# Performance work log

Measured on AMD Instinct MI355X. Metric: run time of the kernel, lower is better.

The kernel has to match this reference:

```python
import jax, jax.numpy as jnp
import numpy as np

LN_EPS = 1e-5


def setup_inputs() -> dict:
    key = jax.random.key(0)
    ks = jax.random.split(key, 8)
    dim = 256
    b, n3 = 8, 6144  # seq dim holds 3 concatenated token streams of n=2048 each
    s = 0.02
    return {
        "x": jax.random.normal(ks[0], (b, n3, dim), jnp.float32),
        "ln_g": jnp.ones((dim,), jnp.float32),
        "ln_b": jnp.zeros((dim,), jnp.float32),
        "Wq": jax.random.normal(ks[1], (dim, dim), jnp.float32) * s,
        "bq": jax.random.normal(ks[2], (dim,), jnp.float32) * s,
        "Wk": jax.random.normal(ks[3], (dim, dim), jnp.float32) * s,
        "bk": jax.random.normal(ks[4], (dim,), jnp.float32) * s,
        "Wv": jax.random.normal(ks[5], (dim, dim), jnp.float32) * s,
        "bv": jax.random.normal(ks[6], (dim,), jnp.float32) * s,
        "Wo": jax.random.normal(ks[7], (dim, dim), jnp.float32) * s,
        "bo": jnp.zeros((dim,), jnp.float32),
        "heads": 8,
    }


def reference(x, ln_g, ln_b, Wq, bq, Wk, bk, Wv, bv, Wo, bo, heads):
    dim = x.shape[-1]
    scale = dim ** (-0.5)  # NOTE: full dim, as in the original module
    d = dim // heads

    def cross_attn(xcat):
        # LayerNorm over last dim (applied to concatenated [2b, n, dim])
        mu = jnp.mean(xcat, axis=-1, keepdims=True)
        var = jnp.mean(jnp.square(xcat - mu), axis=-1, keepdims=True)
        xn = (xcat - mu) * jax.lax.rsqrt(var + LN_EPS) * ln_g + ln_b
        x1, x2 = jnp.split(xn, 2, axis=0)  # queries from stream 1, kv from stream 2
        q = x1 @ Wq.T + bq
        k = x2 @ Wk.T + bk
        v = x2 @ Wv.T + bv
        b_, n_ = q.shape[0], q.shape[1]
        q = q.reshape(b_, n_, heads, d).transpose(0, 2, 1, 3)  # b h n d
        k = k.reshape(b_, n_, heads, d).transpose(0, 2, 1, 3)
        v = v.reshape(b_, n_, heads, d).transpose(0, 2, 1, 3)
        dots = jnp.einsum('bhid,bhjd->bhij', q, k) * scale
        attn = jax.nn.softmax(dots, axis=-1)
        out = jnp.einsum('bhij,bhjd->bhid', attn, v)
        out = out.transpose(0, 2, 1, 3).reshape(b_, n_, dim)
        return out @ Wo.T + bo  # dropout is identity in eval

    x_origin, x_emap, x_lbp = jnp.split(x, 3, axis=1)
    out_oe = cross_attn(jnp.concatenate((x_origin, x_emap), axis=0))
    out_ol = cross_attn(jnp.concatenate((x_origin, x_lbp), axis=0))
    return out_oe + out_ol
```

## Files before the change

### kernel.cpp

```cpp
#include <hip/hip_runtime.h>
#include <hip/hip_bf16.h>
#include <math.h>

#define LN_EPS 1e-5f
#define QSCALE 0.09016844005556021f

typedef __attribute__((ext_vector_type(8))) short short8;
typedef __attribute__((ext_vector_type(4))) short short4v;
typedef __attribute__((ext_vector_type(4))) float f32x4;

__device__ inline ushort f2bf(float f) {
  __hip_bfloat16 h = __float2bfloat16(f);
  return *reinterpret_cast<ushort*>(&h);
}

__device__ inline uint pk2bf(float a, float b) {
  uint ua = __float_as_uint(a) + 0x8000u;
  uint ub = __float_as_uint(b) + 0x8000u;
  return __builtin_amdgcn_perm(ub, ua, 0x07060302u);
}


__global__ __launch_bounds__(256) void ln_wcast_kernel(
    const float* __restrict__ x, const float* __restrict__ lng,
    const float* __restrict__ lnb,
    const float* __restrict__ Wq, const float* __restrict__ Wk,
    const float* __restrict__ Wv, const float* __restrict__ Wo,
    ushort* __restrict__ xn, ushort* __restrict__ wbf) {
  if (blockIdx.x < 256) {
    int t = blockIdx.x * 256 + threadIdx.x;
    int e0 = t * 4;
    int m = e0 >> 16, off = e0 & 65535;
    const float* src = (m == 0) ? Wq : (m == 1) ? Wk : (m == 2) ? Wv : Wo;
    float4 v = *(const float4*)(src + off);
    ushort4 o;
    o.x = f2bf(v.x); o.y = f2bf(v.y); o.z = f2bf(v.z); o.w = f2bf(v.w);
    *(ushort4*)(wbf + m * 65536 + off) = o;
    return;
  }
  int w = threadIdx.x >> 6;
  int lane = threadIdx.x & 63;
  size_t token = (size_t)(blockIdx.x - 256) * 4 + w;
  float4 v = *(const float4*)(x + token * 256 + lane * 4);
  float s  = v.x + v.y + v.z + v.w;
  float s2 = v.x * v.x + v.y * v.y + v.z * v.z + v.w * v.w;
#pragma unroll
  for (int off = 32; off >= 1; off >>= 1) {
    s  += __shfl_xor(s, off, 64);
    s2 += __shfl_xor(s2, off, 64);
  }
  float mu  = s * (1.0f / 256.0f);
  float var = s2 * (1.0f / 256.0f) - mu * mu;
  float rs  = rsqrtf(var + LN_EPS);
  float4 g = *(const float4*)(lng + lane * 4);
  float4 bb = *(const float4*)(lnb + lane * 4);
  ushort4 o;
  o.x = f2bf((v.x - mu) * rs * g.x + bb.x);
  o.y = f2bf((v.y - mu) * rs * g.y + bb.y);
  o.z = f2bf((v.z - mu) * rs * g.z + bb.z);
  o.w = f2bf((v.w - mu) * rs * g.w + bb.w);
  *(ushort4*)(xn + token * 256 + lane * 4) = o;
}

__global__ __launch_bounds__(256) void proj_kernel(
    const ushort* __restrict__ xn,
    const ushort* __restrict__ wq, const ushort* __restrict__ wk,
    const ushort* __restrict__ wv,
    const float* __restrict__ bq, const float* __restrict__ bk,
    const float* __restrict__ bv,
    ushort* __restrict__ qb, ushort* __restrict__ keb, ushort* __restrict__ vTe,
    ushort* __restrict__ klb, ushort* __restrict__ vTl) {
  int z = blockIdx.z;
  const ushort* W; const float* bias; ushort* out; int s; bool isV; float scl;
  if (z == 0)      { W = wq; bias = bq; out = qb;  s = 0; isV = false; scl = QSCALE; }
  else if (z == 1) { W = wk; bias = bk; out = keb; s = 1; isV = false; scl = 1.0f; }
  else if (z == 2) { W = wv; bias = bv; out = vTe; s = 1; isV = true;  scl = 1.0f; }
  else if (z == 3) { W = wk; bias = bk; out = klb; s = 2; isV = false; scl = 1.0f; }
  else             { W = wv; bias = bv; out = vTl; s = 2; isV = true;  scl = 1.0f; }

  int tid = threadIdx.x;
  int w = tid >> 6, lane = tid & 63;
  int n = lane & 15, quad = lane >> 4;
  int cbase = blockIdx.y * 128 + w * 32;

  short8 wfrag[2][8];
#pragma unroll
  for (int ct = 0; ct < 2; ++ct)
#pragma unroll
    for (int kc = 0; kc < 8; ++kc)
      wfrag[ct][kc] = *(const short8*)(W + (size_t)(cbase + ct * 16 + n) * 256 + kc * 32 + quad * 8);
  float4 bt[2]; float bsc[2];
  if (!isV) {
    bt[0] = *(const float4*)(bias + cbase + quad * 4);
    bt[1] = *(const float4*)(bias + cbase + 16 + quad * 4);
  } else {
    bsc[0] = bias[cbase + n];
    bsc[1] = bias[cbase + 16 + n];
  }

  for (int tt = 0; tt < 8; ++tt) {
    int t0 = blockIdx.x * 128 + tt * 16;
    int tok = t0 + n;
    int b = tok >> 11, n2 = tok & 2047;
    const ushort* xrow = xn + ((size_t)b * 6144 + s * 2048 + n2) * 256;
    short8 xf[8];
#pragma unroll
    for (int kc = 0; kc < 8; ++kc)
      xf[kc] = *(const short8*)(xrow + kc * 32 + quad * 8);
    f32x4 acc[2] = {{0.f, 0.f, 0.f, 0.f}, {0.f, 0.f, 0.f, 0.f}};
#pragma unroll
    for (int ct = 0; ct < 2; ++ct)
#pragma unroll
      for (int kc = 0; kc < 8; ++kc)
        acc[ct] = isV
          ? __builtin_amdgcn_mfma_f32_16x16x32_bf16(xf[kc], wfrag[ct][kc], acc[ct], 0, 0, 0)
          : __builtin_amdgcn_mfma_f32_16x16x32_bf16(wfrag[ct][kc], xf[kc], acc[ct], 0, 0, 0);

    if (!isV) {
#pragma unroll
      for (int ct = 0; ct < 2; ++ct) {
        int c = cbase + ct * 16 + quad * 4;
        int h = c >> 5, d = c & 31;
        float* bp = (float*)&bt[ct];
        ushort4 st;
        st.x = f2bf((acc[ct][0] + bp[0]) * scl);
        st.y = f2bf((acc[ct][1] + bp[1]) * scl);
        st.z = f2bf((acc[ct][2] + bp[2]) * scl);
        st.w = f2bf((acc[ct][3] + bp[3]) * scl);
        *(ushort4*)(out + (((size_t)(b * 8 + h) * 2048) + n2) * 32 + d) = st;
      }
    } else {
      int tq0 = t0 + quad * 4;
      int b2 = tq0 >> 11, n2q = tq0 & 2047;
#pragma unroll
      for (int ct = 0; ct < 2; ++ct) {
        int c = cbase + ct * 16 + n;
        int h = c >> 5, d = c & 31;
        ushort4 st;
        st.x = f2bf(acc[ct][0] + bsc[ct]);
        st.y = f2bf(acc[ct][1] + bsc[ct]);
        st.z = f2bf(acc[ct][2] + bsc[ct]);
        st.w = f2bf(acc[ct][3] + bsc[ct]);
        *(ushort4*)(out + (((size_t)(b2 * 8 + h) * 32) + d) * 2048 + n2q) = st;
      }
    }
  }
}

__global__ __launch_bounds__(256) void attn_kernel(
    const ushort* __restrict__ q,
    const ushort* __restrict__ ke, const ushort* __restrict__ vTe,
    const ushort* __restrict__ kl, const ushort* __restrict__ vTl,
    ushort* __restrict__ osum) {
  __shared__ __align__(16) short Vt[4][32 * 72];

  int tid = threadIdx.x;
  int w = tid >> 6, lane = tid & 63;
  int n = lane & 15, quad = lane >> 4;
  short* VtW = &Vt[w][0];

  int L = blockIdx.y * 8 + blockIdx.x;
  int xcd = L & 7, idx = L >> 3;
  int bh = (idx & 7) * 8 + xcd;
  int q0 = (idx >> 3) * 256;
  int qbase = q0 + w * 64;

  short8 qfrag[4];
#pragma unroll
  for (int gq = 0; gq < 4; ++gq)
    qfrag[gq] = *(const short8*)(q + ((size_t)bh * 2048 + qbase + gq * 16 + n) * 32 + quad * 8);

  f32x4 out_acc[4][2];
#pragma unroll
  for (int gq = 0; gq < 4; ++gq)
#pragma unroll
    for (int dh = 0; dh < 2; ++dh) out_acc[gq][dh] = (f32x4){0.f, 0.f, 0.f, 0.f};

  int vrow = lane >> 3, vcol = (lane & 7) * 8;

  for (int s = 0; s < 2; ++s) {
    const ushort* K  = (s == 0 ? ke : kl) + (size_t)bh * 2048 * 32;
    const ushort* VT = (s == 0 ? vTe : vTl) + (size_t)bh * 32 * 2048;
    float lp[4] = {0.f, 0.f, 0.f, 0.f};
    f32x4 oacc[4][2];
#pragma unroll
    for (int gq = 0; gq < 4; ++gq)
#pragma unroll
      for (int dh = 0; dh < 2; ++dh) oacc[gq][dh] = (f32x4){0.f, 0.f, 0.f, 0.f};

    short8 kfc[4], vrc[4], kfn[4], vrn[4];
#pragma unroll
    for (int t4 = 0; t4 < 4; ++t4)
      kfc[t4] = *(const short8*)(K + (size_t)(t4 * 16 + n) * 32 + quad * 8);
#pragma unroll
    for (int it = 0; it < 4; ++it)
      vrc[it] = *(const short8*)(VT + (size_t)(it * 8 + vrow) * 2048 + vcol);

    for (int jt = 0; jt < 32; ++jt) {
      if (jt < 31) {
        int ktn = (jt + 1) * 64;
#pragma unroll
        for (int t4 = 0; t4 < 4; ++t4)
          kfn[t4] = *(const short8*)(K + (size_t)(ktn + t4 * 16 + n) * 32 + quad * 8);
#pragma unroll
        for (int it = 0; it < 4; ++it)
          vrn[it] = *(const short8*)(VT + (size_t)(it * 8 + vrow) * 2048 + ktn + vcol);
      }
#pragma unroll
      for (int it = 0; it < 4; ++it)
        *(short8*)&VtW[(it * 8 + vrow) * 72 + vcol] = vrc[it];
      short4v vbf[2][4];
#pragma unroll
      for (int dh = 0; dh < 2; ++dh)
#pragma unroll
        for (int t4 = 0; t4 < 4; ++t4)
          vbf[dh][t4] = *(const short4v*)&VtW[(dh * 16 + n) * 72 + t4 * 16 + quad * 4];

#pragma unroll
      for (int gq = 0; gq < 4; ++gq) {
        f32x4 sacc[4];
#pragma unroll
        for (int t4 = 0; t4 < 4; ++t4) {
          f32x4 z = {0.f, 0.f, 0.f, 0.f};
          sacc[t4] = __builtin_amdgcn_mfma_f32_16x16x32_bf16(kfc[t4], qfrag[gq], z, 0, 0, 0);
        }
        short4v pf[4];
#pragma unroll
        for (int t4 = 0; t4 < 4; ++t4) {
          float p0 = __builtin_amdgcn_exp2f(sacc[t4][0]);
          float p1 = __builtin_amdgcn_exp2f(sacc[t4][1]);
          float p2 = __builtin_amdgcn_exp2f(sacc[t4][2]);
          float p3 = __builtin_amdgcn_exp2f(sacc[t4][3]);
          lp[gq] += (p0 + p1) + (p2 + p3);
          union { uint2 u; short4v s4; } cv;
          cv.u.x = pk2bf(p0, p1);
          cv.u.y = pk2bf(p2, p3);
          pf[t4] = cv.s4;
        }
#pragma unroll
        for (int t4 = 0; t4 < 4; ++t4)
#pragma unroll
          for (int dh = 0; dh < 2; ++dh)
            oacc[gq][dh] = __builtin_amdgcn_mfma_f32_16x16x16bf16_1k(
                pf[t4], vbf[dh][t4], oacc[gq][dh], 0, 0, 0);
      }
#pragma unroll
      for (int t4 = 0; t4 < 4; ++t4) { kfc[t4] = kfn[t4]; }
#pragma unroll
      for (int it = 0; it < 4; ++it) { vrc[it] = vrn[it]; }
    }
#pragma unroll
    for (int gq = 0; gq < 4; ++gq) {
      float l = lp[gq];
      l += __shfl_xor(l, 16, 64);
      l += __shfl_xor(l, 32, 64);
      float inv = 1.0f / l;
      f32x4 linv;
#pragma unroll
      for (int r = 0; r < 4; ++r) linv[r] = __shfl(inv, quad * 4 + r, 64);
#pragma unroll
      for (int dh = 0; dh < 2; ++dh)
        out_acc[gq][dh] += oacc[gq][dh] * linv;
    }
  }

  int b = bh >> 3, h = bh & 7;
#pragma unroll
  for (int gq = 0; gq < 4; ++gq)
#pragma unroll
    for (int dh = 0; dh < 2; ++dh) {
      f32x4 v = out_acc[gq][dh];
#pragma unroll
      for (int r = 0; r < 4; ++r) {
        size_t row = (size_t)b * 2048 + qbase + gq * 16 + quad * 4 + r;
        osum[row * 256 + h * 32 + dh * 16 + n] = f2bf(v[r]);
      }
    }
}

__global__ __launch_bounds__(256) void outproj_kernel(
    const ushort* __restrict__ osum, const ushort* __restrict__ wo,
    const float* __restrict__ bo, float* __restrict__ out) {
  int tid = threadIdx.x;
  int w = tid >> 6, lane = tid & 63;
  int n = lane & 15, quad = lane >> 4;
  int cbase = blockIdx.y * 128 + w * 32;

  short8 wfrag[2][8];
#pragma unroll
  for (int ct = 0; ct < 2; ++ct)
#pragma unroll
    for (int kc = 0; kc < 8; ++kc)
      wfrag[ct][kc] = *(const short8*)(wo + (size_t)(cbase + ct * 16 + n) * 256 + kc * 32 + quad * 8);
  float4 bt[2];
  bt[0] = *(const float4*)(bo + cbase + quad * 4);
  bt[1] = *(const float4*)(bo + cbase + 16 + quad * 4);

  for (int tt = 0; tt < 8; ++tt) {
    int t0 = blockIdx.x * 128 + tt * 16;
    int tok = t0 + n;
    const ushort* arow = osum + (size_t)tok * 256;
    short8 xf[8];
#pragma unroll
    for (int kc = 0; kc < 8; ++kc)
      xf[kc] = *(const short8*)(arow + kc * 32 + quad * 8);
    f32x4 acc[2] = {{0.f, 0.f, 0.f, 0.f}, {0.f, 0.f, 0.f, 0.f}};
#pragma unroll
    for (int ct = 0; ct < 2; ++ct)
#pragma unroll
      for (int kc = 0; kc < 8; ++kc)
        acc[ct] = __builtin_amdgcn_mfma_f32_16x16x32_bf16(wfrag[ct][kc], xf[kc], acc[ct], 0, 0, 0);
#pragma unroll
    for (int ct = 0; ct < 2; ++ct) {
      int c = cbase + ct * 16 + quad * 4;
      float* bp = (float*)&bt[ct];
      float4 st;
      st.x = acc[ct][0] + 2.0f * bp[0];
      st.y = acc[ct][1] + 2.0f * bp[1];
      st.z = acc[ct][2] + 2.0f * bp[2];
      st.w = acc[ct][3] + 2.0f * bp[3];
      *(float4*)(out + (size_t)tok * 256 + c) = st;
    }
  }
}

extern "C" void kernel_launch(void* const* d_in, const int* in_sizes, int n_in,
                              void* d_out, int out_size, void* d_ws, size_t ws_size,
                              hipStream_t stream) {
  const float* x   = (const float*)d_in[0];
  const float* lng = (const float*)d_in[1];
  const float* lnb = (const float*)d_in[2];
  const float* Wq  = (const float*)d_in[3];
  const float* bq  = (const float*)d_in[4];
  const float* Wk  = (const float*)d_in[5];
  const float* bk  = (const float*)d_in[6];
  const float* Wv  = (const float*)d_in[7];
  const float* bv  = (const float*)d_in[8];
  const float* Wo  = (const float*)d_in[9];
  const float* bo  = (const float*)d_in[10];
  float* out = (float*)d_out;

  ushort* ws = (ushort*)d_ws;
  const size_t XN  = (size_t)49152 * 256;
  const size_t QKV = (size_t)64 * 2048 * 32;
  ushort* xn   = ws;
  ushort* wbf  = xn + XN;
  ushort* qb   = wbf + 4 * 65536;
  ushort* keb  = qb  + QKV;
  ushort* vTe  = keb + QKV;
  ushort* klb  = vTe + QKV;
  ushort* vTl  = klb + QKV;
  ushort* osum = vTl + QKV;

  hipLaunchKernelGGL(ln_wcast_kernel, dim3(12544), dim3(256), 0, stream,
                     x, lng, lnb, Wq, Wk, Wv, Wo, xn, wbf);
  hipLaunchKernelGGL(proj_kernel, dim3(128, 2, 5), dim3(256), 0, stream,
                     xn, wbf, wbf + 65536, wbf + 131072, bq, bk, bv,
                     qb, keb, vTe, klb, vTl);
  hipLaunchKernelGGL(attn_kernel, dim3(8, 64), dim3(256), 0, stream,
                     qb, keb, vTe, klb, vTl, osum);
  hipLaunchKernelGGL(outproj_kernel, dim3(128, 2), dim3(256), 0, stream,
                     osum, wbf + 196608, bo, out);
}
```

Measured before the change: 314.4 us.

## Fuse K/V projections, tile V layout, MFMA row-sum, prefetch activations

The projection kernel now computes K and V for a stream in one block, so each activation tile is read once for both projections, and the grid shrinks from 5 to 3 z-slices. V is stored in 64-token tiles so attention reads each key tile contiguously. The softmax denominator is now computed by an extra MFMA against a ones vector, which replaces the scalar adds and shuffles. Projection and output-projection kernels also double-buffer their activation loads. The extra MFMA per tile and the higher register pressure from doubled weight fragments could reduce occupancy.

New measurement: 289.2 us. 8.0% less time.

```diff
diff --git a/kernel.cpp b/kernel.cpp
--- a/kernel.cpp
+++ b/kernel.cpp
@@ -71,77 +71,125 @@
     ushort* __restrict__ qb, ushort* __restrict__ keb, ushort* __restrict__ vTe,
     ushort* __restrict__ klb, ushort* __restrict__ vTl) {
   int z = blockIdx.z;
-  const ushort* W; const float* bias; ushort* out; int s; bool isV; float scl;
-  if (z == 0)      { W = wq; bias = bq; out = qb;  s = 0; isV = false; scl = QSCALE; }
-  else if (z == 1) { W = wk; bias = bk; out = keb; s = 1; isV = false; scl = 1.0f; }
-  else if (z == 2) { W = wv; bias = bv; out = vTe; s = 1; isV = true;  scl = 1.0f; }
-  else if (z == 3) { W = wk; bias = bk; out = klb; s = 2; isV = false; scl = 1.0f; }
-  else             { W = wv; bias = bv; out = vTl; s = 2; isV = true;  scl = 1.0f; }
-
   int tid = threadIdx.x;
   int w = tid >> 6, lane = tid & 63;
   int n = lane & 15, quad = lane >> 4;
   int cbase = blockIdx.y * 128 + w * 32;
-
-  short8 wfrag[2][8];
-#pragma unroll
-  for (int ct = 0; ct < 2; ++ct)
+  int b = (blockIdx.x * 128) >> 11;
+  int r0 = (blockIdx.x * 128) & 2047;
+
+  if (z == 0) {
+    const ushort* xbase = xn + ((size_t)b * 6144 + r0) * 256;
+    short8 wf[2][8];
+#pragma unroll
+    for (int ct = 0; ct < 2; ++ct)
+#pragma unroll
+      for (int kc = 0; kc < 8; ++kc)
+        wf[ct][kc] = *(const short8*)(wq + (size_t)(cbase + ct * 16 + n) * 256 + kc * 32 + quad * 8);
+    float4 bt[2];
+    bt[0] = *(const float4*)(bq + cbase + quad * 4);
+    bt[1] = *(const float4*)(bq + cbase + 16 + quad * 4);
+
+    short8 xfA[8], xfB[8];
 #pragma unroll
     for (int kc = 0; kc < 8; ++kc)
-      wfrag[ct][kc] = *(const short8*)(W + (size_t)(cbase + ct * 16 + n) * 256 + kc * 32 + quad * 8);
-  float4 bt[2]; float bsc[2];
-  if (!isV) {
-    bt[0] = *(const float4*)(bias + cbase + quad * 4);
-    bt[1] = *(const float4*)(bias + cbase + 16 + quad * 4);
-  } else {
-    bsc[0] = bias[cbase + n];
-    bsc[1] = bias[cbase + 16 + n];
-  }
-
-  for (int tt = 0; tt < 8; ++tt) {
-    int t0 = blockIdx.x * 128 + tt * 16;
-    int tok = t0 + n;
-    int b = tok >> 11, n2 = tok & 2047;
-    const ushort* xrow = xn + ((size_t)b * 6144 + s * 2048 + n2) * 256;
-    short8 xf[8];
-#pragma unroll
-    for (int kc = 0; kc < 8; ++kc)
-      xf[kc] = *(const short8*)(xrow + kc * 32 + quad * 8);
-    f32x4 acc[2] = {{0.f, 0.f, 0.f, 0.f}, {0.f, 0.f, 0.f, 0.f}};
-#pragma unroll
-    for (int ct = 0; ct < 2; ++ct)
-#pragma unroll
-      for (int kc = 0; kc < 8; ++kc)
-        acc[ct] = isV
-          ? __builtin_amdgcn_mfma_f32_16x16x32_bf16(xf[kc], wfrag[ct][kc], acc[ct], 0, 0, 0)
-          : __builtin_amdgcn_mfma_f32_16x16x32_bf16(wfrag[ct][kc], xf[kc], acc[ct], 0, 0, 0);
-
-    if (!isV) {
+      xfA[kc] = *(const short8*)(xbase + (size_t)n * 256 + kc * 32 + quad * 8);
+
+#pragma unroll
+    for (int tt = 0; tt < 8; ++tt) {
+      const short8* cur = (tt & 1) ? xfB : xfA;
+      short8* nxt = (tt & 1) ? xfA : xfB;
+      if (tt < 7) {
+#pragma unroll
+        for (int kc = 0; kc < 8; ++kc)
+          nxt[kc] = *(const short8*)(xbase + (size_t)((tt + 1) * 16 + n) * 256 + kc * 32 + quad * 8);
+      }
+      f32x4 acc[2] = {{0.f, 0.f, 0.f, 0.f}, {0.f, 0.f, 0.f, 0.f}};
+#pragma unroll
+      for (int ct = 0; ct < 2; ++ct)
+#pragma unroll
+        for (int kc = 0; kc < 8; ++kc)
+          acc[ct] = __builtin_amdgcn_mfma_f32_16x16x32_bf16(wf[ct][kc], cur[kc], acc[ct], 0, 0, 0);
+      int n2 = r0 + tt * 16 + n;
 #pragma unroll
       for (int ct = 0; ct < 2; ++ct) {
         int c = cbase + ct * 16 + quad * 4;
         int h = c >> 5, d = c & 31;
         float* bp = (float*)&bt[ct];
         ushort4 st;
-        st.x = f2bf((acc[ct][0] + bp[0]) * scl);
-        st.y = f2bf((acc[ct][1] + bp[1]) * scl);
-        st.z = f2bf((acc[ct][2] + bp[2]) * scl);
-        st.w = f2bf((acc[ct][3] + bp[3]) * scl);
-        *(ushort4*)(out + (((size_t)(b * 8 + h) * 2048) + n2) * 32 + d) = st;
-      }
-    } else {
-      int tq0 = t0 + quad * 4;
-      int b2 = tq0 >> 11, n2q = tq0 & 2047;
+        st.x = f2bf((acc[ct][0] + bp[0]) * QSCALE);
+        st.y = f2bf((acc[ct][1] + bp[1]) * QSCALE);
+        st.z = f2bf((acc[ct][2] + bp[2]) * QSCALE);
+        st.w = f2bf((acc[ct][3] + bp[3]) * QSCALE);
+        *(ushort4*)(qb + (((size_t)(b * 8 + h) * 2048) + n2) * 32 + d) = st;
+      }
+    }
+  } else {
+    int s = z;
+    ushort* kout = (z == 1) ? keb : klb;
+    ushort* vout = (z == 1) ? vTe : vTl;
+    const ushort* xbase = xn + ((size_t)b * 6144 + s * 2048 + r0) * 256;
+    short8 wfk[2][8], wfv[2][8];
+#pragma unroll
+    for (int ct = 0; ct < 2; ++ct)
+#pragma unroll
+      for (int kc = 0; kc < 8; ++kc) {
+        wfk[ct][kc] = *(const short8*)(wk + (size_t)(cbase + ct * 16 + n) * 256 + kc * 32 + quad * 8);
+        wfv[ct][kc] = *(const short8*)(wv + (size_t)(cbase + ct * 16 + n) * 256 + kc * 32 + quad * 8);
+      }
+    float4 btk[2];
+    btk[0] = *(const float4*)(bk + cbase + quad * 4);
+    btk[1] = *(const float4*)(bk + cbase + 16 + quad * 4);
+    float bsv[2] = {bv[cbase + n], bv[cbase + 16 + n]};
+
+    short8 xfA[8], xfB[8];
+#pragma unroll
+    for (int kc = 0; kc < 8; ++kc)
+      xfA[kc] = *(const short8*)(xbase + (size_t)n * 256 + kc * 32 + quad * 8);
+
+#pragma unroll
+    for (int tt = 0; tt < 8; ++tt) {
+      const short8* cur = (tt & 1) ? xfB : xfA;
+      short8* nxt = (tt & 1) ? xfA : xfB;
+      if (tt < 7) {
+#pragma unroll
+        for (int kc = 0; kc < 8; ++kc)
+          nxt[kc] = *(const short8*)(xbase + (size_t)((tt + 1) * 16 + n) * 256 + kc * 32 + quad * 8);
+      }
+      f32x4 ack[2] = {{0.f, 0.f, 0.f, 0.f}, {0.f, 0.f, 0.f, 0.f}};
+      f32x4 acv[2] = {{0.f, 0.f, 0.f, 0.f}, {0.f, 0.f, 0.f, 0.f}};
+#pragma unroll
+      for (int ct = 0; ct < 2; ++ct)
+#pragma unroll
+        for (int kc = 0; kc < 8; ++kc) {
+          ack[ct] = __builtin_amdgcn_mfma_f32_16x16x32_bf16(wfk[ct][kc], cur[kc], ack[ct], 0, 0, 0);
+          acv[ct] = __builtin_amdgcn_mfma_f32_16x16x32_bf16(cur[kc], wfv[ct][kc], acv[ct], 0, 0, 0);
+        }
+      int n2 = r0 + tt * 16 + n;
+#pragma unroll
+      for (int ct = 0; ct < 2; ++ct) {
+        int c = cbase + ct * 16 + quad * 4;
+        int h = c >> 5, d = c & 31;
+        float* bp = (float*)&btk[ct];
+        ushort4 st;
+        st.x = f2bf(ack[ct][0] + bp[0]);
+        st.y = f2bf(ack[ct][1] + bp[1]);
+        st.z = f2bf(ack[ct][2] + bp[2]);
+        st.w = f2bf(ack[ct][3] + bp[3]);
+        *(ushort4*)(kout + (((size_t)(b * 8 + h) * 2048) + n2) * 32 + d) = st;
+      }
+      int tq = r0 + tt * 16 + quad * 4;
+      int tile = tq >> 6, within = tq & 63;
 #pragma unroll
       for (int ct = 0; ct < 2; ++ct) {
         int c = cbase + ct * 16 + n;
         int h = c >> 5, d = c & 31;
         ushort4 st;
-        st.x = f2bf(acc[ct][0] + bsc[ct]);
-        st.y = f2bf(acc[ct][1] + bsc[ct]);
-        st.z = f2bf(acc[ct][2] + bsc[ct]);
-        st.w = f2bf(acc[ct][3] + bsc[ct]);
-        *(ushort4*)(out + (((size_t)(b2 * 8 + h) * 32) + d) * 2048 + n2q) = st;
+        st.x = f2bf(acv[ct][0] + bsv[ct]);
+        st.y = f2bf(acv[ct][1] + bsv[ct]);
+        st.z = f2bf(acv[ct][2] + bsv[ct]);
+        st.w = f2bf(acv[ct][3] + bsv[ct]);
+        *(ushort4*)(vout + (size_t)(b * 8 + h) * 65536 + tile * 2048 + d * 64 + within) = st;
       }
     }
   }
@@ -159,6 +207,10 @@
   int n = lane & 15, quad = lane >> 4;
   short* VtW = &Vt[w][0];
 
+  union { uint2 u; short4v s; } one_u;
+  one_u.u.x = 0x3F803F80u; one_u.u.y = 0x3F803F80u;
+  const short4v vone = one_u.s;
+
   int L = blockIdx.y * 8 + blockIdx.x;
   int xcd = L & 7, idx = L >> 3;
   int bh = (idx & 7) * 8 + xcd;
@@ -181,12 +233,14 @@
   for (int s = 0; s < 2; ++s) {
     const ushort* K  = (s == 0 ? ke : kl) + (size_t)bh * 2048 * 32;
     const ushort* VT = (s == 0 ? vTe : vTl) + (size_t)bh * 32 * 2048;
-    float lp[4] = {0.f, 0.f, 0.f, 0.f};
+    f32x4 lacc[4];
     f32x4 oacc[4][2];
 #pragma unroll
-    for (int gq = 0; gq < 4; ++gq)
+    for (int gq = 0; gq < 4; ++gq) {
+      lacc[gq] = (f32x4){0.f, 0.f, 0.f, 0.f};
 #pragma unroll
       for (int dh = 0; dh < 2; ++dh) oacc[gq][dh] = (f32x4){0.f, 0.f, 0.f, 0.f};
+    }
 
     short8 kfc[4], vrc[4], kfn[4], vrn[4];
 #pragma unroll
@@ -194,17 +248,17 @@
       kfc[t4] = *(const short8*)(K + (size_t)(t4 * 16 + n) * 32 + quad * 8);
 #pragma unroll
     for (int it = 0; it < 4; ++it)
-      vrc[it] = *(const short8*)(VT + (size_t)(it * 8 + vrow) * 2048 + vcol);
+      vrc[it] = *(const short8*)(VT + it * 512 + vrow * 64 + vcol);
 
     for (int jt = 0; jt < 32; ++jt) {
       if (jt < 31) {
-        int ktn = (jt + 1) * 64;
+        size_t tb = (size_t)(jt + 1) * 2048;
 #pragma unroll
         for (int t4 = 0; t4 < 4; ++t4)
-          kfn[t4] = *(const short8*)(K + (size_t)(ktn + t4 * 16 + n) * 32 + quad * 8);
+          kfn[t4] = *(const short8*)(K + tb + (size_t)(t4 * 16 + n) * 32 + quad * 8);
 #pragma unroll
         for (int it = 0; it < 4; ++it)
-          vrn[it] = *(const short8*)(VT + (size_t)(it * 8 + vrow) * 2048 + ktn + vcol);
+          vrn[it] = *(const short8*)(VT + tb + it * 512 + vrow * 64 + vcol);
       }
 #pragma unroll
       for (int it = 0; it < 4; ++it)
@@ -231,18 +285,20 @@
           float p1 = __builtin_amdgcn_exp2f(sacc[t4][1]);
           float p2 = __builtin_amdgcn_exp2f(sacc[t4][2]);
           float p3 = __builtin_amdgcn_exp2f(sacc[t4][3]);
-          lp[gq] += (p0 + p1) + (p2 + p3);
           union { uint2 u; short4v s4; } cv;
           cv.u.x = pk2bf(p0, p1);
           cv.u.y = pk2bf(p2, p3);
           pf[t4] = cv.s4;
         }
 #pragma unroll
-        for (int t4 = 0; t4 < 4; ++t4)
-#pragma unroll
-          for (int dh = 0; dh < 2; ++dh)
-            oacc[gq][dh] = __builtin_amdgcn_mfma_f32_16x16x16bf16_1k(
-                pf[t4], vbf[dh][t4], oacc[gq][dh], 0, 0, 0);
+        for (int t4 = 0; t4 < 4; ++t4) {
+          oacc[gq][0] = __builtin_amdgcn_mfma_f32_16x16x16bf16_1k(
+              pf[t4], vbf[0][t4], oacc[gq][0], 0, 0, 0);
+          oacc[gq][1] = __builtin_amdgcn_mfma_f32_16x16x16bf16_1k(
+              pf[t4], vbf[1][t4], oacc[gq][1], 0, 0, 0);
+          lacc[gq] = __builtin_amdgcn_mfma_f32_16x16x16bf16_1k(
+              pf[t4], vone, lacc[gq], 0, 0, 0);
+        }
       }
 #pragma unroll
       for (int t4 = 0; t4 < 4; ++t4) { kfc[t4] = kfn[t4]; }
@@ -251,16 +307,12 @@
     }
 #pragma unroll
     for (int gq = 0; gq < 4; ++gq) {
-      float l = lp[gq];
-      l += __shfl_xor(l, 16, 64);
-      l += __shfl_xor(l, 32, 64);
-      float inv = 1.0f / l;
-      f32x4 linv;
-#pragma unroll
-      for (int r = 0; r < 4; ++r) linv[r] = __shfl(inv, quad * 4 + r, 64);
+      f32x4 inv;
+#pragma unroll
+      for (int r = 0; r < 4; ++r) inv[r] = __builtin_amdgcn_rcpf(lacc[gq][r]);
 #pragma unroll
       for (int dh = 0; dh < 2; ++dh)
-        out_acc[gq][dh] += oacc[gq][dh] * linv;
+        out_acc[gq][dh] += oacc[gq][dh] * inv;
     }
   }
 
@@ -296,20 +348,28 @@
   bt[0] = *(const float4*)(bo + cbase + quad * 4);
   bt[1] = *(const float4*)(bo + cbase + 16 + quad * 4);
 
+  const ushort* abase = osum + (size_t)(blockIdx.x * 128) * 256;
+  short8 xfA[8], xfB[8];
+#pragma unroll
+  for (int kc = 0; kc < 8; ++kc)
+    xfA[kc] = *(const short8*)(abase + (size_t)n * 256 + kc * 32 + quad * 8);
+
+#pragma unroll
   for (int tt = 0; tt < 8; ++tt) {
-    int t0 = blockIdx.x * 128 + tt * 16;
-    int tok = t0 + n;
-    const ushort* arow = osum + (size_t)tok * 256;
-    short8 xf[8];
-#pragma unroll
-    for (int kc = 0; kc < 8; ++kc)
-      xf[kc] = *(const short8*)(arow + kc * 32 + quad * 8);
+    const short8* cur = (tt & 1) ? xfB : xfA;
+    short8* nxt = (tt & 1) ? xfA : xfB;
+    if (tt < 7) {
+#pragma unroll
+      for (int kc = 0; kc < 8; ++kc)
+        nxt[kc] = *(const short8*)(abase + (size_t)((tt + 1) * 16 + n) * 256 + kc * 32 + quad * 8);
+    }
+    int tok = blockIdx.x * 128 + tt * 16 + n;
     f32x4 acc[2] = {{0.f, 0.f, 0.f, 0.f}, {0.f, 0.f, 0.f, 0.f}};
 #pragma unroll
     for (int ct = 0; ct < 2; ++ct)
 #pragma unroll
       for (int kc = 0; kc < 8; ++kc)
-        acc[ct] = __builtin_amdgcn_mfma_f32_16x16x32_bf16(wfrag[ct][kc], xf[kc], acc[ct], 0, 0, 0);
+        acc[ct] = __builtin_amdgcn_mfma_f32_16x16x32_bf16(wfrag[ct][kc], cur[kc], acc[ct], 0, 0, 0);
 #pragma unroll
     for (int ct = 0; ct < 2; ++ct) {
       int c = cbase + ct * 16 + quad * 4;
@@ -354,7 +414,7 @@
 
   hipLaunchKernelGGL(ln_wcast_kernel, dim3(12544), dim3(256), 0, stream,
                      x, lng, lnb, Wq, Wk, Wv, Wo, xn, wbf);
-  hipLaunchKernelGGL(proj_kernel, dim3(128, 2, 5), dim3(256), 0, stream,
+  hipLaunchKernelGGL(proj_kernel, dim3(128, 2, 3), dim3(256), 0, stream,
                      xn, wbf, wbf + 65536, wbf + 131072, bq, bk, bv,
                      qb, keb, vTe, klb, vTl);
   hipLaunchKernelGGL(attn_kernel, dim3(8, 64), dim3(256), 0, stream,
```
